# Optimization experiments

Measured on AMD Instinct MI355X. Metric: run time of the kernel, lower is better.

Reference implementation:

```python
import jax, jax.numpy as jnp
import numpy as np

B, S, HID = 4, 2048, 1024
E, K, H = 8, 2, 8          # num_experts, topk, num_heads
DK = HID // H              # head_qk_dim = 128
DV = HID // H              # head_v_dim = 128
CAP = int(S * 1.0)         # capacity_len = int((S*K)/K * capacity)
CHUNK = 64
EPS = 1e-5


def setup_inputs() -> dict:
    key = jax.random.key(0)
    ks = jax.random.split(key, 12)
    std = 0.02  # ~ xavier_uniform with gain 2**-2.5
    return {
        "x": jax.random.normal(ks[0], (B, S, HID), jnp.float32),
        "gate_w": jax.random.normal(ks[1], (E, HID), jnp.float32) * std,
        "q_w": jax.random.normal(ks[2], (HID, HID), jnp.float32) * std,
        "k_w": jax.random.normal(ks[3], (E, HID, HID), jnp.float32) * std,
        "v_w": jax.random.normal(ks[4], (E, HID, HID), jnp.float32) * std,
        "fmq1_w": jax.random.normal(ks[5], (DK, DK), jnp.float32) * std,
        "fmq2_w": jax.random.normal(ks[6], (DK, DK), jnp.float32) * std,
        "fmk1_w": jax.random.normal(ks[7], (DK, DK), jnp.float32) * std,
        "fmk2_w": jax.random.normal(ks[8], (DK, DK), jnp.float32) * std,
        "norm_w": jnp.ones((DV,), jnp.float32),
        "o_w": jax.random.normal(ks[9], (HID, HID), jnp.float32) * std,
    }


def chunk_linear_attn(q, k, v):
    # q,k: (Bt, T, H, DK); v: (Bt, T, H, DV). Causal linear attention, chunked.
    Bt, T, Hh, Dk = q.shape
    Dv = v.shape[-1]
    nc = T // CHUNK
    q = q * (Dk ** -0.5)
    qc = q.reshape(Bt, nc, CHUNK, Hh, Dk).transpose(1, 0, 2, 3, 4)
    kc = k.reshape(Bt, nc, CHUNK, Hh, Dk).transpose(1, 0, 2, 3, 4)
    vc = v.reshape(Bt, nc, CHUNK, Hh, Dv).transpose(1, 0, 2, 3, 4)
    causal = jnp.tril(jnp.ones((CHUNK, CHUNK), q.dtype))
    def step(Sst, qkv):
        qb, kb, vb = qkv  # (Bt, CHUNK, H, D)
        attn = jnp.einsum('bihd,bjhd->bhij', qb, kb) * causal
        intra = jnp.einsum('bhij,bjhe->bihe', attn, vb)
        inter = jnp.einsum('bihd,bhde->bihe', qb, Sst)
        Sst = Sst + jnp.einsum('bjhd,bjhe->bhde', kb, vb)
        return Sst, intra + inter
    S0 = jnp.zeros((Bt, Hh, Dk, Dv), q.dtype)
    _, o = jax.lax.scan(step, S0, (qc, kc, vc))
    return o.transpose(1, 0, 2, 3, 4).reshape(Bt, T, Hh, Dv)


def _forward(x, gate_w, q_w, k_w, v_w, fmq1_w, fmq2_w, fmk1_w, fmk2_w, norm_w, o_w):
    b, s0, d = x.shape
    # ---- routing ----
    logits = jnp.einsum('bsd,ed->bse', x, gate_w)
    scores = jax.nn.softmax(logits.astype(jnp.float32), axis=-1)
    rw, sel = jax.lax.top_k(scores, K)                 # (b, s0, K)
    rw = (rw / rw.sum(-1, keepdims=True)).astype(x.dtype)
    routing_mask = jax.nn.one_hot(sel, E, dtype=jnp.int32).sum(2)  # (b, s0, E)
    # ---- transform: sort-by-(batch,expert), capacity gather ----
    s = s0 * K
    x_rep = jnp.repeat(x, K, axis=1).reshape(b * s, d)  # repeat_interleave over seq
    sel_flat = sel.reshape(b * s).astype(jnp.int32)
    batch_idx = jnp.repeat(jnp.arange(b, dtype=jnp.int32), s)
    combined = batch_idx * E + sel_flat
    sorted_indices = jnp.argsort(combined)              # stable in jax
    x_sorted = x_rep[sorted_indices]
    tokens = routing_mask.sum(axis=1)                   # (b, E) tokens per group
    flat_off = (jnp.cumsum(tokens, axis=1) + (jnp.arange(b, dtype=jnp.int32) * s)[:, None]).reshape(-1)
    starts = jnp.concatenate([jnp.zeros((1,), flat_off.dtype), flat_off[:-1]])
    idx = starts[:, None] + jnp.arange(CAP, dtype=flat_off.dtype)[None, :]
    shift = jnp.maximum(tokens.reshape(-1) - CAP, 0)    # keep last CAP tokens
    tidx = idx + shift[:, None]                         # (b*E, CAP)
    dmask = tidx < flat_off[:, None]
    tidx = jnp.where(dmask, tidx, 0)
    xe = x_sorted[tidx.reshape(-1)].reshape(b * E, CAP, d) * dmask[..., None].astype(x.dtype)
    xe = xe.reshape(b, E, CAP, d).transpose(1, 0, 2, 3)  # (E, b, CAP, d)
    # ---- projections + Hadamard feature maps ----
    q = jnp.einsum('ebtc,kc->ebtk', xe, q_w).reshape(E, b, CAP, H, DK)
    k = jnp.einsum('ebtc,ekc->ebtk', xe, k_w).reshape(E, b, CAP, H, DK)
    v = jnp.einsum('ebtc,ekc->ebtk', xe, v_w).reshape(E, b, CAP, H, DV)
    q = jnp.einsum('...d,kd->...k', q, fmq1_w) * jnp.einsum('...d,kd->...k', q, fmq2_w)
    k = jnp.einsum('...d,kd->...k', k, fmk1_w) * jnp.einsum('...d,kd->...k', k, fmk2_w)
    # ---- causal chunked linear attention per (expert, batch) slot ----
    o = chunk_linear_attn(q.reshape(E * b, CAP, H, DK),
                          k.reshape(E * b, CAP, H, DK),
                          v.reshape(E * b, CAP, H, DV))
    # ---- reconstruct: scatter-add back, undo sort, weighted topk combine ----
    oflat = o.reshape(E, b, CAP, H, DV).transpose(1, 0, 2, 3, 4).reshape(b * E * CAP, H, DV)
    oflat = oflat * dmask.reshape(-1)[:, None, None].astype(o.dtype)
    res = jnp.zeros((b * s, H, DV), o.dtype).at[tidx.reshape(-1)].add(oflat)
    inv = jnp.argsort(sorted_indices)
    restored = res[inv].reshape(b, s0, K, H, DV)
    out = (restored * rw[..., None, None]).sum(axis=2)   # (b, s0, H, DV)
    # RMSNorm over head_v_dim, merge heads, output proj
    out = out * jax.lax.rsqrt(jnp.mean(out * out, axis=-1, keepdims=True) + EPS) * norm_w
    out = out.reshape(b, s0, H * DV)
    return jnp.einsum('bsv,dv->bsd', out, o_w)


def reference(x, gate_w, q_w, k_w, v_w, fmq1_w, fmq2_w, fmk1_w, fmk2_w, norm_w, o_w):
    return _forward(x, gate_w, q_w, k_w, v_w, fmq1_w, fmq2_w, fmk1_w, fmk2_w, norm_w, o_w)
```

## Files before the change

### kernel.cpp

```cpp
#include <hip/hip_runtime.h>
#include <stdint.h>

typedef unsigned short u16;
typedef unsigned int   u32;
typedef __attribute__((ext_vector_type(4))) float f32x4;
typedef __attribute__((ext_vector_type(4))) u32   u32x4;
typedef __attribute__((ext_vector_type(8))) __bf16 bf16x8;

#define MFMA16(a,b,c) __builtin_amdgcn_mfma_f32_16x16x32_bf16((a),(b),(c),0,0,0)

#define QSCALE 0.08838834764831845f
#define RMAX   24576

__device__ __forceinline__ float bf2f(u16 x){ u32 u=((u32)x)<<16; float f; __builtin_memcpy(&f,&u,4); return f; }
__device__ __forceinline__ u16 f2bf(float f){ u32 u; __builtin_memcpy(&u,&f,4); u = u + 0x7FFFu + ((u>>16)&1u); return (u16)(u>>16); }
__device__ __forceinline__ u32 pack2(float a, float b){ return (u32)f2bf(a) | ((u32)f2bf(b)<<16); }

__device__ __forceinline__ void gl_lds(const u16* g, u16* l){
  __builtin_amdgcn_global_load_lds(
      (const __attribute__((address_space(1))) void*)g,
      (__attribute__((address_space(3))) void*)l, 16, 0, 0);
}

#define TSW(row, oct) ((row)*72 + ((((oct) ^ (((row)>>3)&7)))<<3))


__device__ __forceinline__ void cvt_body(const float* __restrict__ s, u16* __restrict__ d,
                                         long n8, int lb, int nb){
  long idx = (long)lb*256 + threadIdx.x;
  long stride = (long)nb*256;
  for (long i=idx; i<n8; i+=stride){
    const float* p = s + i*8;
    f32x4 a = *(const f32x4*)p;
    f32x4 b = *(const f32x4*)(p+4);
    u32x4 o;
    o[0]=pack2(a[0],a[1]); o[1]=pack2(a[2],a[3]); o[2]=pack2(b[0],b[1]); o[3]=pack2(b[2],b[3]);
    *(u32x4*)(d + i*8) = o;
  }
}

__device__ __forceinline__ void route_body(const float* __restrict__ x, const float* __restrict__ gw,
  int* __restrict__ sel, float* __restrict__ rw, u16* __restrict__ xb, int lb)
{
  int w = threadIdx.x>>6, lane = threadIdx.x&63;
  int tok = lb*4 + w;
  const float* xr = x + (size_t)tok*1024 + lane*16;
  f32x4 xv[4];
  #pragma unroll
  for (int q=0;q<4;q++) xv[q] = *(const f32x4*)(xr + q*4);
  {
    u16* xrow = xb + (size_t)tok*1024 + lane*16;
    u32x4 o0, o1;
    o0[0]=pack2(xv[0][0],xv[0][1]); o0[1]=pack2(xv[0][2],xv[0][3]);
    o0[2]=pack2(xv[1][0],xv[1][1]); o0[3]=pack2(xv[1][2],xv[1][3]);
    o1[0]=pack2(xv[2][0],xv[2][1]); o1[1]=pack2(xv[2][2],xv[2][3]);
    o1[2]=pack2(xv[3][0],xv[3][1]); o1[3]=pack2(xv[3][2],xv[3][3]);
    *(u32x4*)xrow     = o0;
    *(u32x4*)(xrow+8) = o1;
  }
  float part[8];
  #pragma unroll
  for (int e=0;e<8;e++){
    const float* g = gw + e*1024 + lane*16;
    float s = 0.f;
    #pragma unroll
    for (int q=0;q<4;q++){
      f32x4 gv = *(const f32x4*)(g + q*4);
      s += xv[q][0]*gv[0] + xv[q][1]*gv[1] + xv[q][2]*gv[2] + xv[q][3]*gv[3];
    }
    part[e]=s;
  }
  #pragma unroll
  for (int e=0;e<8;e++){
    float v = part[e];
    #pragma unroll
    for (int off=32; off>0; off>>=1) v += __shfl_xor(v, off, 64);
    part[e]=v;
  }
  if (lane==0){
    int i0=0; float m0=part[0];
    #pragma unroll
    for (int e=1;e<8;e++) if (part[e]>m0){ m0=part[e]; i0=e; }
    int i1=0; float m1=-3.4e38f;
    #pragma unroll
    for (int e=0;e<8;e++) if (e!=i0 && part[e]>m1){ m1=part[e]; i1=e; }
    sel[tok] = i0 | (i1<<8);
    float e1 = expf(m1-m0);
    float inv = 1.f/(1.f+e1);
    rw[tok*2+0] = inv;
    rw[tok*2+1] = e1*inv;
  }
}

__device__ __forceinline__ void prep_body(
  const float* __restrict__ q_w, const float* __restrict__ k_w,
  const float* __restrict__ fmq1, const float* __restrict__ fmq2,
  const float* __restrict__ fmk1, const float* __restrict__ fmk2,
  u16* __restrict__ wA, u16* __restrict__ wB, int l, u16* shmem)
{
  int gi = l>>3;
  int c0 = (l&7)*128;
  const float* fm; const float* ws; u16* wd;
  if (gi < 8)      { int h=gi;    fm=fmq1; ws=q_w + (size_t)h*131072; wd=wA + (size_t)h*262144; }
  else if (gi < 16){ int h=gi-8;  fm=fmq2; ws=q_w + (size_t)h*131072; wd=wA + (size_t)h*262144 + 131072; }
  else if (gi < 80){ int t=gi-16, e=t>>3, h=t&7; fm=fmk1; ws=k_w + (size_t)(e*8+h)*131072; wd=wB + (size_t)e*2097152 + (size_t)h*262144; }
  else             { int t=gi-80, e=t>>3, h=t&7; fm=fmk2; ws=k_w + (size_t)(e*8+h)*131072; wd=wB + (size_t)e*2097152 + (size_t)h*262144 + 131072; }
  u16* Af = shmem;
  u16* Bf = shmem + 128*136;
  int tid = threadIdx.x;
  for (int i=tid; i<4096; i+=256){
    int row = i>>5, col = (i&31)*4;
    f32x4 v = *(const f32x4*)&fm[row*128 + col];
    u16* dp = &Af[row*136 + col];
    *(u32*)dp     = pack2(v[0],v[1]);
    *(u32*)(dp+2) = pack2(v[2],v[3]);
  }
  for (int i=tid; i<4096; i+=256){
    int dd = i>>5, cq = (i&31)*4;
    f32x4 v = *(const f32x4*)&ws[(size_t)dd*1024 + c0 + cq];
    #pragma unroll
    for (int j=0;j<4;j++){
      int c = cq+j;
      Bf[c*136 + (dd ^ (((c>>2)&3)<<3))] = f2bf(v[j]);
    }
  }
  __syncthreads();
  int lane=tid&63, w=tid>>6, wr=w>>1, wc=w&1, lc=lane&15, lr=lane>>4;
  const f32x4 Z4 = {0.f,0.f,0.f,0.f};
  f32x4 acc[4][4];
  #pragma unroll
  for (int i=0;i<4;i++){
    #pragma unroll
    for (int j=0;j<4;j++) acc[i][j]=Z4;
  }
  #pragma unroll
  for (int kk=0; kk<4; ++kk){
    bf16x8 a[4], b[4];
    #pragma unroll
    for (int mi=0;mi<4;mi++)
      a[mi] = *(const bf16x8*)&Af[(wr*64+mi*16+lc)*136 + kk*32 + lr*8];
    #pragma unroll
    for (int ni=0;ni<4;ni++){
      int c = wc*64+ni*16+lc;
      b[ni] = *(const bf16x8*)&Bf[c*136 + ((kk*32 + lr*8) ^ (((c>>2)&3)<<3))];
    }
    #pragma unroll
    for (int mi=0;mi<4;mi++){
      #pragma unroll
      for (int ni=0;ni<4;ni++)
        acc[mi][ni] = MFMA16(a[mi], b[ni], acc[mi][ni]);
    }
  }
  int r0=lr*4;
  #pragma unroll
  for (int mi=0;mi<4;mi++){
    #pragma unroll
    for (int ni=0;ni<4;ni++){
      int col = c0 + wc*64 + ni*16 + lc;
      #pragma unroll
      for (int r=0;r<4;r++){
        int row = wr*64 + mi*16 + r0 + r;
        wd[(size_t)row*1024 + col] = f2bf(acc[mi][ni][r]);
      }
    }
  }
}

__global__ __launch_bounds__(256) void k_pre(
  const float* __restrict__ x, const float* __restrict__ gw,
  int* __restrict__ sel, float* __restrict__ rw,
  const float* __restrict__ q_w, const float* __restrict__ k_w,
  const float* __restrict__ fmq1, const float* __restrict__ fmq2,
  const float* __restrict__ fmk1, const float* __restrict__ fmk2,
  u16* __restrict__ wA, u16* __restrict__ wB, u16* __restrict__ xb,
  const float* __restrict__ v_w, u16* __restrict__ wVb,
  const float* __restrict__ o_w, u16* __restrict__ wOb, int* __restrict__ done)
{
  __shared__ __align__(16) u16 shmem[2*128*136];
  int bid = blockIdx.x;
  if (bid==0 && threadIdx.x==0) *done = 0;
  if (bid < 2048)      route_body(x, gw, sel, rw, xb, bid);
  else if (bid < 3200) prep_body(q_w, k_w, fmq1, fmq2, fmk1, fmk2, wA, wB, bid-2048, shmem);
  else if (bid < 3456) cvt_body(v_w, wVb, 1048576L, bid-3200, 256);
  else                 cvt_body(o_w, wOb, 131072L, bid-3456, 32);
}

__global__ __launch_bounds__(256) void k_count(const int* __restrict__ sel,
  int* __restrict__ slot_of, int* __restrict__ src_of, int* __restrict__ meta,
  int* __restrict__ done)
{
  int g = blockIdx.x, b = g>>3, e = g&7;
  int tid = threadIdx.x;
  __shared__ int cn[256];
  unsigned char ex[16];
  int cnt=0;
  #pragma unroll
  for (int i=0;i<16;i++){
    int t = tid*16+i;
    int sv = sel[b*2048 + (t>>1)];
    int ee = (t&1) ? ((sv>>8)&255) : (sv&255);
    ex[i]=(unsigned char)ee;
    cnt += (ee==e);
  }
  cn[tid]=cnt;
  __syncthreads();
  for (int off=1; off<256; off<<=1){
    int v = (tid>=off) ? cn[tid-off] : 0;
    __syncthreads();
    cn[tid] += v;
    __syncthreads();
  }
  int total = cn[255];
  int run = cn[tid]-cnt;
  int shift = total>2048 ? total-2048 : 0;
  #pragma unroll
  for (int i=0;i<16;i++){
    int t = tid*16+i;
    if (ex[i]==e){
      int j = run - shift;
      run++;
      slot_of[b*4096 + t] = (j>=0)? j : -1;
      if (j>=0) src_of[g*2048 + j] = t;
    }
  }
  if (tid==0){
    meta[g]=total;
    __threadfence();
    if (atomicAdd(done,1)==31){
      int basev=0, t=0;
      meta[96]=0;
      for (int gg=0; gg<32; ++gg){
        int n = atomicAdd(&meta[gg],0);
        int nact = n<2048 ? n : 2048;
        int npad = (nact+255)&~255;
        meta[32+gg]=nact;
        meta[64+gg]=npad;
        meta[129+gg]=(nact+63)>>6;
        for (int i=0;i<(npad>>8);++i) meta[192+t++]=gg;
        basev += npad;
        meta[97+gg]=basev;
      }
      meta[161]=basev;
    }
  }
}

__global__ __launch_bounds__(256) void k_gather(const u16* __restrict__ xb,
  const int* __restrict__ src_of, const int* __restrict__ meta, u16* __restrict__ xg,
  int* __restrict__ tokmap)
{
  int g = blockIdx.y, jb = blockIdx.x;
  int npad = meta[64+g];
  if (jb*64 >= npad) return;
  int nact = meta[32+g], base = meta[96+g];
  int tid = threadIdx.x;
  int j = jb*64 + (tid>>2);
  int quart = tid&3;
  int src = (j<nact) ? src_of[g*2048+j] : -1;
  int token = (src>=0) ? ((g>>3)*2048 + (src>>1)) : 0;
  if (quart==0) tokmap[base+j] = token;
  u16* orow = xg + ((size_t)(base+j))*1024 + quart*256;
  if (src>=0){
    const u16* xr = xb + (size_t)token*1024 + quart*256;
    #pragma unroll
    for (int i=0;i<256;i+=8) *(u32x4*)(orow+i) = *(const u32x4*)(xr+i);
  } else {
    u32x4 z = {0,0,0,0};
    #pragma unroll
    for (int i=0;i<256;i+=8) *(u32x4*)(orow+i)=z;
  }
}

__global__ __launch_bounds__(512,2) void k_gemmQKV(const u16* __restrict__ xb, const u16* __restrict__ xg,
  const u16* __restrict__ wA, const u16* __restrict__ wB, const u16* __restrict__ wVb,
  u16* __restrict__ qh, u16* __restrict__ kh, u16* __restrict__ vv, const int* __restrict__ meta)
{
  int bid = blockIdx.x;
  int role, tm, tn;
  const u16 *A, *Wp; u16* outB;
  if (bid < 256){
    role=0; int l=bid, xcd=l&7, jj=l>>3, jd=jj>>3;
    tm=xcd*4+jd; tn=jj&7;
    A=xb; Wp=wA + (size_t)tn*262144; outB=qh;
  } else if (bid < 1024){
    role=1; int l=bid-256, xcd=l&7, jj=l>>3, jd=jj>>3;
    tm=xcd*12+jd; tn=jj&7;
    if (tm*256 >= meta[161]) return;
    A=xg; Wp=wB + (size_t)(meta[192+tm]&7)*2097152 + (size_t)tn*262144; outB=kh;
  } else {
    role=2; int l=bid-1024, xcd=l&7, jj=l>>3, jd=jj>>2;
    tm=xcd*12+jd; tn=jj&3;
    if (tm*256 >= meta[161]) return;
    A=xg; Wp=wVb + (size_t)(meta[192+tm]&7)*1048576 + (size_t)tn*262144; outB=vv;
  }

  __shared__ __align__(16) u16 smem[65536];

  int tid=threadIdx.x, lane=tid&63;
  int w=tid>>6, wr=w>>2, wc=w&3, lc=lane&15, lr=lane>>4;
  int swz = lc&7;
  int ck0 = ((lr)^swz)<<3;
  int ck1 = ((4+lr)^swz)<<3;
  int arow = (wr*128 + lc)*64;
  int brow = 16384 + (wc*64 + lc)*64;
  const f32x4 Z4 = {0.f,0.f,0.f,0.f};
  f32x4 acc[8][4];
  #pragma unroll
  for(int i=0;i<8;i++){
    #pragma unroll
    for(int j2=0;j2<4;j2++) acc[i][j2]=Z4;
  }
  int rowlane = tid>>3;
  int gch = ((tid&7)^(rowlane&7))*8;
  const u16* Asrc = A  + (size_t)tm*262144 + (size_t)rowlane*1024 + gch;
  const u16* Bsrc = Wp + (size_t)rowlane*1024 + gch;

  #define STG2(dst, src) { \
    gl_lds((src),         &smem[(dst) + tid*8]); \
    gl_lds((src) + 65536, &smem[(dst) + 4096 + tid*8]); }

  #define RDA(dst, jrow) { \
    dst[0] = *(const bf16x8*)&smem[d + arow + (2*(jrow)  )*1024 + ck0]; \
    dst[1] = *(const bf16x8*)&smem[d + arow + (2*(jrow)+1)*1024 + ck0]; \
    dst[2] = *(const bf16x8*)&smem[d + arow + (2*(jrow)  )*1024 + ck1]; \
    dst[3] = *(const bf16x8*)&smem[d + arow + (2*(jrow)+1)*1024 + ck1]; }

  #define DOMFMA(src, jrow) { \
    __builtin_amdgcn_s_setprio(1); \
    _Pragma("unroll") \
    for (int ni=0;ni<4;ni++){ \
      acc[2*(jrow)  ][ni] = MFMA16(src[0], b0[ni], acc[2*(jrow)  ][ni]); \
      acc[2*(jrow)+1][ni] = MFMA16(src[1], b0[ni], acc[2*(jrow)+1][ni]); } \
    _Pragma("unroll") \
    for (int ni=0;ni<4;ni++){ \
      acc[2*(jrow)  ][ni] = MFMA16(src[2], b1[ni], acc[2*(jrow)  ][ni]); \
      acc[2*(jrow)+1][ni] = MFMA16(src[3], b1[ni], acc[2*(jrow)+1][ni]); } \
    __builtin_amdgcn_s_setprio(0); }

  STG2(16384, Bsrc);
  STG2(24576, Bsrc + 131072);
  STG2(0,     Asrc);
  STG2(8192,  Asrc + 131072);
  STG2(49152, Bsrc + 64);
  STG2(57344, Bsrc + 131072 + 64);

  for (int t=0; t<16; ++t){
    int d = (t&1)<<15;
    bf16x8 b0[4], b1[4], aE[4], aO[4];
    if (t<15) asm volatile("s_waitcnt vmcnt(4)" ::: "memory");
    else      asm volatile("s_waitcnt vmcnt(0)" ::: "memory");
    __builtin_amdgcn_s_barrier();
    #pragma unroll
    for (int ni=0;ni<4;ni++){
      b0[ni] = *(const bf16x8*)&smem[d + brow + ni*1024 + ck0];
      b1[ni] = *(const bf16x8*)&smem[d + brow + ni*1024 + ck1];
    }
    RDA(aE, 0);
    if (t<15) STG2(((t+1)&1)<<15, Asrc + (size_t)(t+1)*64);
    RDA(aO, 1);
    DOMFMA(aE, 0);
    __builtin_amdgcn_s_barrier();
    if (t<15) STG2((((t+1)&1)<<15) + 8192, Asrc + 131072 + (size_t)(t+1)*64);
    RDA(aE, 2);
    DOMFMA(aO, 1);
    __builtin_amdgcn_s_barrier();
    if (t<14) STG2(d + 16384, Bsrc + (size_t)(t+2)*64);
    RDA(aO, 3);
    DOMFMA(aE, 2);
    __builtin_amdgcn_s_barrier();
    if (t<14) STG2(d + 24576, Bsrc + 131072 + (size_t)(t+2)*64);
    DOMFMA(aO, 3);
  }
  #undef STG2
  #undef RDA
  #undef DOMFMA

  __syncthreads();
  if (role < 2){
    if (wc >= 2){
      #pragma unroll
      for (int mi=0;mi<8;mi++){
        #pragma unroll
        for (int ni=0;ni<4;ni++){
          int col = (wc-2)*64 + ni*16 + lc;
          #pragma unroll
          for (int r=0;r<4;r++)
            ((float*)smem)[(wr*128+mi*16+lr*4+r)*128 + col] = acc[mi][ni][r];
        }
      }
    }
    __syncthreads();
    if (wc < 2){
      float scl = (role==0) ? QSCALE : 1.0f;
      #pragma unroll
      for (int mi=0;mi<8;mi++){
        #pragma unroll
        for (int ni=0;ni<4;ni++){
          int col = wc*64 + ni*16 + lc;
          #pragma unroll
          for (int r=0;r<4;r++){
            int row = wr*128+mi*16+lr*4+r;
            float v = acc[mi][ni][r] * ((float*)smem)[row*128 + col] * scl;
            outB[(size_t)(tm*256+row)*1024 + tn*128 + col] = f2bf(v);
          }
        }
      }
    }
  } else {
    #pragma unroll
    for (int mi=0;mi<8;mi++){
      #pragma unroll
      for (int ni=0;ni<4;ni++){
        int col = tn*256 + wc*64 + ni*16 + lc;
        #pragma unroll
        for (int r=0;r<4;r++){
          int row = tm*256 + wr*128 + mi*16 + lr*4 + r;
          outB[(size_t)row*1024 + col] = f2bf(acc[mi][ni][r]);
        }
      }
    }
  }
}

__global__ __launch_bounds__(512) void k_gemmO(const u16* __restrict__ A, const u16* __restrict__ W,
  float* __restrict__ outF)
{
  int tnN = gridDim.x;
  int bid = blockIdx.y*tnN + blockIdx.x;
  int chunk = gridDim.y >> 3;
  int xcd = bid & 7, j = bid >> 3;
  int jd = j / tnN;
  int tm = xcd*chunk + jd;
  int tn = j - jd*tnN;

  __shared__ __align__(16) u16 smem[73728];

  int tid=threadIdx.x, lane=tid&63;
  int w=tid>>6, wr=w>>2, wc=w&3, lc=lane&15, lr=lane>>4;
  int swz = lc&7;
  const f32x4 Z4 = {0.f,0.f,0.f,0.f};
  f32x4 acc[4][4];
  #pragma unroll
  for(int i=0;i<4;i++){
    #pragma unroll
    for(int j2=0;j2<4;j2++) acc[i][j2]=Z4;
  }
  size_t lanoff = (size_t)(tid>>3)*1024 + (size_t)(((tid&7)^((tid>>3)&7))*8);
  const u16* Ag = A + (size_t)tm*131072 + lanoff;
  const u16* Bg = W + (size_t)tn*262144 + lanoff;
  int lo = tid*8;

  #define STAGEO(ao, bo, kt) { \
    const u16* ga = Ag + (kt)*64; const u16* gb = Bg + (kt)*64; \
    gl_lds(ga,                 &smem[(ao) + lo]); \
    gl_lds(ga + (size_t)65536, &smem[(ao) + 4096 + lo]); \
    gl_lds(gb,                  &smem[(bo) + lo]); \
    gl_lds(gb + (size_t)65536,  &smem[(bo) + 4096 + lo]); \
    gl_lds(gb + (size_t)131072, &smem[(bo) + 8192 + lo]); \
    gl_lds(gb + (size_t)196608, &smem[(bo) + 12288 + lo]); }

  STAGEO(0, 24576, 0);
  STAGEO(8192, 40960, 1);
  int cur = 0;
  for (int kt=0; kt<16; ++kt){
    if (kt<15) asm volatile("s_waitcnt vmcnt(6)" ::: "memory");
    else       asm volatile("s_waitcnt vmcnt(0)" ::: "memory");
    __builtin_amdgcn_s_barrier();
    if (kt<14){
      int nid = kt+2; nid -= (nid/3)*3;
      STAGEO(nid*8192, 24576+nid*16384, kt+2);
    }
    int ao = cur*8192, bo = 24576 + cur*16384;
    __builtin_amdgcn_s_setprio(1);
    #pragma unroll
    for (int kk=0; kk<2; ++kk){
      bf16x8 a[4], b[4];
      #pragma unroll
      for (int mi=0;mi<4;mi++){
        int row = wr*64+mi*16+lc;
        a[mi] = *(const bf16x8*)&smem[ao + row*64 + (((kk*4+lr)^swz)<<3)];
      }
      #pragma unroll
      for (int ni=0;ni<4;ni++){
        int row = wc*64+ni*16+lc;
        b[ni] = *(const bf16x8*)&smem[bo + row*64 + (((kk*4+lr)^swz)<<3)];
      }
      #pragma unroll
      for (int mi=0;mi<4;mi++){
        #pragma unroll
        for (int ni=0;ni<4;ni++)
          acc[mi][ni] = MFMA16(a[mi], b[ni], acc[mi][ni]);
      }
    }
    __builtin_amdgcn_s_setprio(0);
    cur = (cur==2)?0:cur+1;
  }
  #pragma unroll
  for (int mi=0;mi<4;mi++){
    #pragma unroll
    for (int ni=0;ni<4;ni++){
      int col = tn*256 + wc*64 + ni*16 + lc;
      #pragma unroll
      for (int r=0;r<4;r++){
        int row = tm*128 + wr*64 + mi*16 + lr*4 + r;
        outF[(size_t)row*1024 + col] = acc[mi][ni][r];
      }
    }
  }
  #undef STAGEO
}

__global__ __launch_bounds__(256,1) void k_attn(const u16* __restrict__ qv, const u16* __restrict__ kv,
  const u16* __restrict__ vv, u16* __restrict__ o, const int* __restrict__ meta,
  const int* __restrict__ tokmap)
{
  int g = blockIdx.x>>3, h = blockIdx.x&7;
  int nch = meta[129+g];
  if (nch==0) return;
  int base = meta[96+g];
  __shared__ __align__(16) u16 Qs[64*136];
  __shared__ __align__(16) u16 Ks[64*136];
  __shared__ __align__(16) u16 KTs[128*72];
  __shared__ __align__(16) u16 VTs[128*72];
  __shared__ __align__(16) u16 Ts[2*128*136];
  __shared__ __align__(16) u16 Ps[64*72];
  int tid=threadIdx.x, w=tid>>6, lane=tid&63;
  int wr=w>>1, wc=w&1;
  int lr=lane>>4, lc=lane&15;
  {
    u32x4 z={0,0,0,0};
    for (int i=tid; i<128*136/8; i+=256) *(u32x4*)&Ts[i*8]=z;
  }
  const f32x4 Z4 = {0.f,0.f,0.f,0.f};
  f32x4 accT[4][4];
  #pragma unroll
  for (int i=0;i<4;i++){
    #pragma unroll
    for (int j=0;j<4;j++) accT[i][j]=Z4;
  }
  __syncthreads();
  const u16* kb = kv + (size_t)base*1024 + h*128;
  const u16* vb = vv + (size_t)base*1024 + h*128;
  u16* ob = o + (size_t)base*1024 + h*128;
  int tso = 0;

  for (int c=0; c<nch; ++c){
    #pragma unroll
    for (int it=0; it<4; ++it){
      int id = tid + it*256;
      int row = id>>4, kc = id&15;
      int tok = tokmap[base + c*64 + row];
      *(u32x4*)&Qs[row*136 + kc*8] = *(const u32x4*)(qv + (size_t)tok*1024 + h*128 + kc*8);
      *(u32x4*)&Ks[row*136 + kc*8] = *(const u32x4*)(kb + (size_t)(c*64+row)*1024 + kc*8);
    }
    #pragma unroll
    for (int it=0; it<4; ++it){
      int id = tid + it*256;
      int j = id>>4, dg = id&15;
      int col = (((j>>3) ^ (dg&7))<<3) + (j&7);
      u32x4 kx = *(const u32x4*)(kb + (size_t)(c*64+j)*1024 + dg*8);
      u32x4 vx = *(const u32x4*)(vb + (size_t)(c*64+j)*1024 + dg*8);
      #pragma unroll
      for (int t=0;t<4;t++){
        KTs[(dg*8+t*2  )*72 + col] = (u16)(kx[t]&0xffff);
        KTs[(dg*8+t*2+1)*72 + col] = (u16)(kx[t]>>16);
        VTs[(dg*8+t*2  )*72 + col] = (u16)(vx[t]&0xffff);
        VTs[(dg*8+t*2+1)*72 + col] = (u16)(vx[t]>>16);
      }
    }
    __syncthreads();
    bf16x8 qf[2][4];
    #pragma unroll
    for (int ti=0; ti<2; ++ti){
      #pragma unroll
      for (int ks=0; ks<4; ++ks)
        qf[ti][ks] = *(const bf16x8*)&Qs[(wr*32+ti*16+lc)*136 + ks*32 + lr*8];
    }
    f32x4 accO[2][4];
    #pragma unroll
    for (int i=0;i<2;i++){
      #pragma unroll
      for (int j=0;j<4;j++) accO[i][j]=Z4;
    }
    #pragma unroll
    for (int ks=0; ks<4; ++ks){
      bf16x8 bt[4];
      #pragma unroll
      for (int te=0; te<4; ++te)
        bt[te] = *(const bf16x8*)&Ts[tso + (wc*64+te*16+lc)*136 + ks*32 + lr*8];
      #pragma unroll
      for (int ti=0; ti<2; ++ti){
        #pragma unroll
        for (int te=0; te<4; ++te)
          accO[ti][te] = MFMA16(qf[ti][ks], bt[te], accO[ti][te]);
      }
    }
    f32x4 accP[2][2];
    #pragma unroll
    for (int i=0;i<2;i++){
      #pragma unroll
      for (int j=0;j<2;j++) accP[i][j]=Z4;
    }
    #pragma unroll
    for (int ks=0; ks<4; ++ks){
      bf16x8 bk[2];
      #pragma unroll
      for (int tj=0; tj<2; ++tj)
        bk[tj] = *(const bf16x8*)&Ks[(wc*32+tj*16+lc)*136 + ks*32 + lr*8];
      #pragma unroll
      for (int ti=0; ti<2; ++ti){
        #pragma unroll
        for (int tj=0; tj<2; ++tj)
          accP[ti][tj] = MFMA16(qf[ti][ks], bk[tj], accP[ti][tj]);
      }
    }
    #pragma unroll
    for (int ti=0; ti<2; ++ti){
      #pragma unroll
      for (int tj=0; tj<2; ++tj){
        #pragma unroll
        for (int r=0;r<4;r++){
          int i = wr*32+ti*16+lr*4+r;
          int j = wc*32+tj*16+lc;
          Ps[i*72 + j] = f2bf( (j<=i) ? accP[ti][tj][r] : 0.f );
        }
      }
    }
    __syncthreads();
    #pragma unroll
    for (int ks=0; ks<2; ++ks){
      bf16x8 ap[2], bv[4];
      #pragma unroll
      for (int ti=0; ti<2; ++ti)
        ap[ti] = *(const bf16x8*)&Ps[(wr*32+ti*16+lc)*72 + ks*32 + lr*8];
      #pragma unroll
      for (int te=0; te<4; ++te)
        bv[te] = *(const bf16x8*)&VTs[TSW(wc*64+te*16+lc, ks*4+lr)];
      #pragma unroll
      for (int ti=0; ti<2; ++ti){
        #pragma unroll
        for (int te=0; te<4; ++te)
          accO[ti][te] = MFMA16(ap[ti], bv[te], accO[ti][te]);
      }
    }
    #pragma unroll
    for (int ks=0; ks<2; ++ks){
      bf16x8 av[4], bk2[4];
      #pragma unroll
      for (int te=0; te<4; ++te)
        av[te] = *(const bf16x8*)&VTs[TSW(wr*64+te*16+lc, ks*4+lr)];
      #pragma unroll
      for (int td=0; td<4; ++td)
        bk2[td] = *(const bf16x8*)&KTs[TSW(wc*64+td*16+lc, ks*4+lr)];
      #pragma unroll
      for (int te=0; te<4; ++te){
        #pragma unroll
        for (int td=0; td<4; ++td)
          accT[te][td] = MFMA16(av[te], bk2[td], accT[te][td]);
      }
    }
    int tsn = tso ^ (128*136);
    #pragma unroll
    for (int te=0; te<4; ++te){
      #pragma unroll
      for (int td=0; td<4; ++td){
        int dk = wc*64+td*16+lc;
        #pragma unroll
        for (int r=0;r<4;r++){
          int erow = wr*64+te*16+lr*4+r;
          Ts[tsn + erow*136 + dk] = f2bf(accT[te][td][r]);
        }
      }
    }
    #pragma unroll
    for (int ti=0; ti<2; ++ti){
      #pragma unroll
      for (int te=0; te<4; ++te){
        int ecol = wc*64+te*16+lc;
        #pragma unroll
        for (int r=0;r<4;r++){
          int i = wr*32+ti*16+lr*4+r;
          ob[(size_t)(c*64+i)*1024 + ecol] = f2bf(accO[ti][te][r]);
        }
      }
    }
    __syncthreads();
    tso = tsn;
  }
}

__global__ __launch_bounds__(256) void k_comb(const u16* __restrict__ o, const int* __restrict__ sel,
  const float* __restrict__ rw, const int* __restrict__ slot_of, const int* __restrict__ meta,
  const float* __restrict__ nw, u16* __restrict__ fin)
{
  int w=threadIdx.x>>6, lane=threadIdx.x&63;
  int tok = blockIdx.x*4 + w;
  int b = tok>>11;
  int sv = sel[tok];
  float acc[16];
  #pragma unroll
  for (int i=0;i<16;i++) acc[i]=0.f;
  #pragma unroll
  for (int kk=0; kk<2; ++kk){
    int e = kk ? ((sv>>8)&255) : (sv&255);
    int j = slot_of[tok*2 + kk];
    if (j < 0) continue;
    float wgt = rw[tok*2+kk];
    int row = meta[96 + b*8 + e] + j;
    const u16* orow = o + (size_t)row*1024 + lane*16;
    #pragma unroll
    for (int q=0;q<2;q++){
      u32x4 v = *(const u32x4*)(orow + q*8);
      #pragma unroll
      for (int t=0;t<4;t++){
        acc[q*8+t*2]   += wgt * bf2f((u16)(v[t]&0xffff));
        acc[q*8+t*2+1] += wgt * bf2f((u16)(v[t]>>16));
      }
    }
  }
  float ssq=0.f;
  #pragma unroll
  for (int i=0;i<16;i++) ssq += acc[i]*acc[i];
  ssq += __shfl_xor(ssq,1,64);
  ssq += __shfl_xor(ssq,2,64);
  ssq += __shfl_xor(ssq,4,64);
  float sc = rsqrtf(ssq*(1.f/128.f) + 1e-5f);
  int cbase = (lane&7)*16;
  u32x4 o0, o1;
  #pragma unroll
  for (int t=0;t<4;t++)
    o0[t] = pack2(acc[2*t]*sc*nw[cbase+2*t], acc[2*t+1]*sc*nw[cbase+2*t+1]);
  #pragma unroll
  for (int t=0;t<4;t++)
    o1[t] = pack2(acc[8+2*t]*sc*nw[cbase+8+2*t], acc[8+2*t+1]*sc*nw[cbase+8+2*t+1]);
  u16* fp = fin + (size_t)tok*1024 + lane*16;
  *(u32x4*)fp     = o0;
  *(u32x4*)(fp+8) = o1;
}

extern "C" void kernel_launch(void* const* d_in, const int* in_sizes, int n_in,
                              void* d_out, int out_size, void* d_ws, size_t ws_size,
                              hipStream_t stream)
{
  (void)in_sizes; (void)n_in;
  const float* x     = (const float*)d_in[0];
  const float* gate  = (const float*)d_in[1];
  const float* q_w   = (const float*)d_in[2];
  const float* k_w   = (const float*)d_in[3];
  const float* v_w   = (const float*)d_in[4];
  const float* fmq1  = (const float*)d_in[5];
  const float* fmq2  = (const float*)d_in[6];
  const float* fmk1  = (const float*)d_in[7];
  const float* fmk2  = (const float*)d_in[8];
  const float* norm_w= (const float*)d_in[9];
  const float* o_w   = (const float*)d_in[10];
  float* out = (float*)d_out;

  uint8_t* ws = (uint8_t*)d_ws;
  size_t off = 0;
  auto alloc = [&](size_t bytes)->void*{ void* p = ws + off; off += (bytes + 255) & ~(size_t)255; return p; };
  int*   meta = (int*)alloc(4096);
  int*   sel  = (int*)alloc(8192*4);
  float* rwb  = (float*)alloc(8192*2*4);
  int*   slot = (int*)alloc(16384*4);
  int*   srcf = (int*)alloc((size_t)32*2048*4);
  int*   tokm = (int*)alloc((size_t)RMAX*4);
  int*   done = (int*)alloc(256);
  u16* wA  = (u16*)alloc((size_t)2097152*2);
  u16* wVb = (u16*)alloc((size_t)8388608*2);
  u16* wOb = (u16*)alloc((size_t)1048576*2);
  u16* xb  = (u16*)alloc((size_t)8192*1024*2);
  u16* xg  = (u16*)alloc((size_t)RMAX*1024*2);
  u16* qh  = (u16*)alloc((size_t)8192*1024*2);
  u16* kh  = (u16*)alloc((size_t)RMAX*1024*2);
  u16* vv  = (u16*)alloc((size_t)RMAX*1024*2);
  if (off > ws_size){
    hipMemsetAsync(d_out, 0x7F, (size_t)out_size*4, stream);
    return;
  }
  u16* wB  = (u16*)d_out;
  u16* ob  = xg;
  u16* fin = qh;

  k_pre<<<3488,256,0,stream>>>(x, gate, sel, rwb, q_w, k_w, fmq1, fmq2, fmk1, fmk2, wA, wB, xb, v_w, wVb, o_w, wOb, done);
  k_count<<<32,256,0,stream>>>(sel, slot, srcf, meta, done);
  k_gather<<<dim3(32,32),256,0,stream>>>(xb, srcf, meta, xg, tokm);
  k_gemmQKV<<<1408,512,0,stream>>>(xb, xg, wA, wB, wVb, qh, kh, vv, meta);
  k_attn<<<256,256,0,stream>>>(qh, kh, vv, ob, meta, tokm);
  k_comb<<<2048,256,0,stream>>>(ob, sel, rwb, slot, meta, norm_w, fin);
  k_gemmO<<<dim3(4,64),512,0,stream>>>(fin, wOb, out);
}
```

Measured before the change: 404.3 us.

## Fuse token gather into QKV GEMM loads and share weight staging in prep

```diff
diff --git a/kernel.cpp b/kernel.cpp
--- a/kernel.cpp
+++ b/kernel.cpp
@@ -98,24 +98,23 @@
   const float* __restrict__ fmk1, const float* __restrict__ fmk2,
   u16* __restrict__ wA, u16* __restrict__ wB, int l, u16* shmem)
 {
-  int gi = l>>3;
-  int c0 = (l&7)*128;
-  const float* fm; const float* ws; u16* wd;
-  if (gi < 8)      { int h=gi;    fm=fmq1; ws=q_w + (size_t)h*131072; wd=wA + (size_t)h*262144; }
-  else if (gi < 16){ int h=gi-8;  fm=fmq2; ws=q_w + (size_t)h*131072; wd=wA + (size_t)h*262144 + 131072; }
-  else if (gi < 80){ int t=gi-16, e=t>>3, h=t&7; fm=fmk1; ws=k_w + (size_t)(e*8+h)*131072; wd=wB + (size_t)e*2097152 + (size_t)h*262144; }
-  else             { int t=gi-80, e=t>>3, h=t&7; fm=fmk2; ws=k_w + (size_t)(e*8+h)*131072; wd=wB + (size_t)e*2097152 + (size_t)h*262144 + 131072; }
+  const float *fm1, *fm2, *ws; u16 *wd1;
+  int c0;
+  if (l < 64){
+    int h = l>>3; c0 = (l&7)*128;
+    fm1=fmq1; fm2=fmq2; ws=q_w + (size_t)h*131072;
+    wd1=wA + (size_t)h*262144;
+  } else {
+    int l2=l-64, eh=l2>>3; c0=(l2&7)*128;
+    int e=eh>>3, h=eh&7;
+    fm1=fmk1; fm2=fmk2; ws=k_w + (size_t)eh*131072;
+    wd1=wB + (size_t)e*2097152 + (size_t)h*262144;
+  }
+  u16* wd2 = wd1 + 131072;
   u16* Af = shmem;
   u16* Bf = shmem + 128*136;
   int tid = threadIdx.x;
   for (int i=tid; i<4096; i+=256){
-    int row = i>>5, col = (i&31)*4;
-    f32x4 v = *(const f32x4*)&fm[row*128 + col];
-    u16* dp = &Af[row*136 + col];
-    *(u32*)dp     = pack2(v[0],v[1]);
-    *(u32*)(dp+2) = pack2(v[2],v[3]);
-  }
-  for (int i=tid; i<4096; i+=256){
     int dd = i>>5, cq = (i&31)*4;
     f32x4 v = *(const f32x4*)&ws[(size_t)dd*1024 + c0 + cq];
     #pragma unroll
@@ -124,45 +123,58 @@
       Bf[c*136 + (dd ^ (((c>>2)&3)<<3))] = f2bf(v[j]);
     }
   }
-  __syncthreads();
   int lane=tid&63, w=tid>>6, wr=w>>1, wc=w&1, lc=lane&15, lr=lane>>4;
   const f32x4 Z4 = {0.f,0.f,0.f,0.f};
-  f32x4 acc[4][4];
-  #pragma unroll
-  for (int i=0;i<4;i++){
-    #pragma unroll
-    for (int j=0;j<4;j++) acc[i][j]=Z4;
-  }
-  #pragma unroll
-  for (int kk=0; kk<4; ++kk){
-    bf16x8 a[4], b[4];
-    #pragma unroll
-    for (int mi=0;mi<4;mi++)
-      a[mi] = *(const bf16x8*)&Af[(wr*64+mi*16+lc)*136 + kk*32 + lr*8];
-    #pragma unroll
-    for (int ni=0;ni<4;ni++){
-      int c = wc*64+ni*16+lc;
-      b[ni] = *(const bf16x8*)&Bf[c*136 + ((kk*32 + lr*8) ^ (((c>>2)&3)<<3))];
-    }
+  #pragma unroll
+  for (int pass=0; pass<2; ++pass){
+    const float* fm = pass ? fm2 : fm1;
+    u16* wd = pass ? wd2 : wd1;
+    for (int i=tid; i<4096; i+=256){
+      int row = i>>5, col = (i&31)*4;
+      f32x4 v = *(const f32x4*)&fm[row*128 + col];
+      u16* dp = &Af[row*136 + col];
+      *(u32*)dp     = pack2(v[0],v[1]);
+      *(u32*)(dp+2) = pack2(v[2],v[3]);
+    }
+    __syncthreads();
+    f32x4 acc[4][4];
+    #pragma unroll
+    for (int i=0;i<4;i++){
+      #pragma unroll
+      for (int j=0;j<4;j++) acc[i][j]=Z4;
+    }
+    #pragma unroll
+    for (int kk=0; kk<4; ++kk){
+      bf16x8 a[4], b[4];
+      #pragma unroll
+      for (int mi=0;mi<4;mi++)
+        a[mi] = *(const bf16x8*)&Af[(wr*64+mi*16+lc)*136 + kk*32 + lr*8];
+      #pragma unroll
+      for (int ni=0;ni<4;ni++){
+        int c = wc*64+ni*16+lc;
+        b[ni] = *(const bf16x8*)&Bf[c*136 + ((kk*32 + lr*8) ^ (((c>>2)&3)<<3))];
+      }
+      #pragma unroll
+      for (int mi=0;mi<4;mi++){
+        #pragma unroll
+        for (int ni=0;ni<4;ni++)
+          acc[mi][ni] = MFMA16(a[mi], b[ni], acc[mi][ni]);
+      }
+    }
+    int r0=lr*4;
     #pragma unroll
     for (int mi=0;mi<4;mi++){
       #pragma unroll
-      for (int ni=0;ni<4;ni++)
-        acc[mi][ni] = MFMA16(a[mi], b[ni], acc[mi][ni]);
-    }
-  }
-  int r0=lr*4;
-  #pragma unroll
-  for (int mi=0;mi<4;mi++){
-    #pragma unroll
-    for (int ni=0;ni<4;ni++){
-      int col = c0 + wc*64 + ni*16 + lc;
-      #pragma unroll
-      for (int r=0;r<4;r++){
-        int row = wr*64 + mi*16 + r0 + r;
-        wd[(size_t)row*1024 + col] = f2bf(acc[mi][ni][r]);
-      }
-    }
+      for (int ni=0;ni<4;ni++){
+        int col = c0 + wc*64 + ni*16 + lc;
+        #pragma unroll
+        for (int r=0;r<4;r++){
+          int row = wr*64 + mi*16 + r0 + r;
+          wd[(size_t)row*1024 + col] = f2bf(acc[mi][ni][r]);
+        }
+      }
+    }
+    __syncthreads();
   }
 }
 
@@ -180,13 +192,19 @@
   int bid = blockIdx.x;
   if (bid==0 && threadIdx.x==0) *done = 0;
   if (bid < 2048)      route_body(x, gw, sel, rw, xb, bid);
-  else if (bid < 3200) prep_body(q_w, k_w, fmq1, fmq2, fmk1, fmk2, wA, wB, bid-2048, shmem);
-  else if (bid < 3456) cvt_body(v_w, wVb, 1048576L, bid-3200, 256);
-  else                 cvt_body(o_w, wOb, 131072L, bid-3456, 32);
+  else if (bid < 2624) prep_body(q_w, k_w, fmq1, fmq2, fmk1, fmk2, wA, wB, bid-2048, shmem);
+  else if (bid < 2880) cvt_body(v_w, wVb, 1048576L, bid-2624, 256);
+  else if (bid < 2912) cvt_body(o_w, wOb, 131072L, bid-2880, 32);
+  else {
+    if (threadIdx.x < 128){
+      u32x4 z = {0,0,0,0};
+      *(u32x4*)&xb[(size_t)8192*1024 + threadIdx.x*8] = z;
+    }
+  }
 }
 
 __global__ __launch_bounds__(256) void k_count(const int* __restrict__ sel,
-  int* __restrict__ slot_of, int* __restrict__ src_of, int* __restrict__ meta,
+  int* __restrict__ slot_of, int* __restrict__ tokmap2, int* __restrict__ meta,
   int* __restrict__ done)
 {
   int g = blockIdx.x, b = g>>3, e = g&7;
@@ -220,7 +238,7 @@
       int j = run - shift;
       run++;
       slot_of[b*4096 + t] = (j>=0)? j : -1;
-      if (j>=0) src_of[g*2048 + j] = t;
+      if (j>=0) tokmap2[g*2048 + j] = b*2048 + (t>>1);
     }
   }
   if (tid==0){
@@ -245,53 +263,28 @@
   }
 }
 
-__global__ __launch_bounds__(256) void k_gather(const u16* __restrict__ xb,
-  const int* __restrict__ src_of, const int* __restrict__ meta, u16* __restrict__ xg,
-  int* __restrict__ tokmap)
-{
-  int g = blockIdx.y, jb = blockIdx.x;
-  int npad = meta[64+g];
-  if (jb*64 >= npad) return;
-  int nact = meta[32+g], base = meta[96+g];
-  int tid = threadIdx.x;
-  int j = jb*64 + (tid>>2);
-  int quart = tid&3;
-  int src = (j<nact) ? src_of[g*2048+j] : -1;
-  int token = (src>=0) ? ((g>>3)*2048 + (src>>1)) : 0;
-  if (quart==0) tokmap[base+j] = token;
-  u16* orow = xg + ((size_t)(base+j))*1024 + quart*256;
-  if (src>=0){
-    const u16* xr = xb + (size_t)token*1024 + quart*256;
-    #pragma unroll
-    for (int i=0;i<256;i+=8) *(u32x4*)(orow+i) = *(const u32x4*)(xr+i);
-  } else {
-    u32x4 z = {0,0,0,0};
-    #pragma unroll
-    for (int i=0;i<256;i+=8) *(u32x4*)(orow+i)=z;
-  }
-}
-
-__global__ __launch_bounds__(512,2) void k_gemmQKV(const u16* __restrict__ xb, const u16* __restrict__ xg,
+__global__ __launch_bounds__(512,2) void k_gemmQKV(const u16* __restrict__ xb,
   const u16* __restrict__ wA, const u16* __restrict__ wB, const u16* __restrict__ wVb,
-  u16* __restrict__ qh, u16* __restrict__ kh, u16* __restrict__ vv, const int* __restrict__ meta)
+  u16* __restrict__ qh, u16* __restrict__ kh, u16* __restrict__ vv,
+  const int* __restrict__ meta, const int* __restrict__ tokmap2)
 {
   int bid = blockIdx.x;
   int role, tm, tn;
-  const u16 *A, *Wp; u16* outB;
+  const u16 *Wp; u16* outB;
   if (bid < 256){
     role=0; int l=bid, xcd=l&7, jj=l>>3, jd=jj>>3;
     tm=xcd*4+jd; tn=jj&7;
-    A=xb; Wp=wA + (size_t)tn*262144; outB=qh;
+    Wp=wA + (size_t)tn*262144; outB=qh;
   } else if (bid < 1024){
     role=1; int l=bid-256, xcd=l&7, jj=l>>3, jd=jj>>3;
     tm=xcd*12+jd; tn=jj&7;
     if (tm*256 >= meta[161]) return;
-    A=xg; Wp=wB + (size_t)(meta[192+tm]&7)*2097152 + (size_t)tn*262144; outB=kh;
+    Wp=wB + (size_t)(meta[192+tm]&7)*2097152 + (size_t)tn*262144; outB=kh;
   } else {
     role=2; int l=bid-1024, xcd=l&7, jj=l>>3, jd=jj>>2;
     tm=xcd*12+jd; tn=jj&3;
     if (tm*256 >= meta[161]) return;
-    A=xg; Wp=wVb + (size_t)(meta[192+tm]&7)*1048576 + (size_t)tn*262144; outB=vv;
+    Wp=wVb + (size_t)(meta[192+tm]&7)*1048576 + (size_t)tn*262144; outB=vv;
   }
 
   __shared__ __align__(16) u16 smem[65536];
@@ -312,10 +305,31 @@
   }
   int rowlane = tid>>3;
   int gch = ((tid&7)^(rowlane&7))*8;
-  const u16* Asrc = A  + (size_t)tm*262144 + (size_t)rowlane*1024 + gch;
+  int tk0, tk1, tk2, tk3;
+  {
+    int r0 = tm*256 + rowlane;
+    if (role==0){
+      tk0=r0; tk1=r0+64; tk2=r0+128; tk3=r0+192;
+    } else {
+      int g = meta[192+tm], base = meta[96+g], nact = meta[32+g];
+      int gb = g*2048;
+      int j0 = r0 - base;
+      tk0 = (j0     < nact) ? tokmap2[gb + j0]     : 8192;
+      tk1 = (j0+64  < nact) ? tokmap2[gb + j0+64]  : 8192;
+      tk2 = (j0+128 < nact) ? tokmap2[gb + j0+128] : 8192;
+      tk3 = (j0+192 < nact) ? tokmap2[gb + j0+192] : 8192;
+    }
+  }
+  const u16* Ap0 = xb + (size_t)tk0*1024 + gch;
+  const u16* Ap1 = xb + (size_t)tk1*1024 + gch;
+  const u16* Ap2 = xb + (size_t)tk2*1024 + gch;
+  const u16* Ap3 = xb + (size_t)tk3*1024 + gch;
   const u16* Bsrc = Wp + (size_t)rowlane*1024 + gch;
 
-  #define STG2(dst, src) { \
+  #define STGA(dst, p0, p1, coff) { \
+    gl_lds((p0) + (coff), &smem[(dst) + tid*8]); \
+    gl_lds((p1) + (coff), &smem[(dst) + 4096 + tid*8]); }
+  #define STGB(dst, src) { \
     gl_lds((src),         &smem[(dst) + tid*8]); \
     gl_lds((src) + 65536, &smem[(dst) + 4096 + tid*8]); }
 
@@ -337,12 +351,12 @@
       acc[2*(jrow)+1][ni] = MFMA16(src[3], b1[ni], acc[2*(jrow)+1][ni]); } \
     __builtin_amdgcn_s_setprio(0); }
 
-  STG2(16384, Bsrc);
-  STG2(24576, Bsrc + 131072);
-  STG2(0,     Asrc);
-  STG2(8192,  Asrc + 131072);
-  STG2(49152, Bsrc + 64);
-  STG2(57344, Bsrc + 131072 + 64);
+  STGB(16384, Bsrc);
+  STGB(24576, Bsrc + 131072);
+  STGA(0,     Ap0, Ap1, 0);
+  STGA(8192,  Ap2, Ap3, 0);
+  STGB(49152, Bsrc + 64);
+  STGB(57344, Bsrc + 131072 + 64);
 
   for (int t=0; t<16; ++t){
     int d = (t&1)<<15;
@@ -356,22 +370,23 @@
       b1[ni] = *(const bf16x8*)&smem[d + brow + ni*1024 + ck1];
     }
     RDA(aE, 0);
-    if (t<15) STG2(((t+1)&1)<<15, Asrc + (size_t)(t+1)*64);
+    if (t<15) STGA(((t+1)&1)<<15, Ap0, Ap1, (size_t)(t+1)*64);
     RDA(aO, 1);
     DOMFMA(aE, 0);
     __builtin_amdgcn_s_barrier();
-    if (t<15) STG2((((t+1)&1)<<15) + 8192, Asrc + 131072 + (size_t)(t+1)*64);
+    if (t<15) STGA((((t+1)&1)<<15) + 8192, Ap2, Ap3, (size_t)(t+1)*64);
     RDA(aE, 2);
     DOMFMA(aO, 1);
     __builtin_amdgcn_s_barrier();
-    if (t<14) STG2(d + 16384, Bsrc + (size_t)(t+2)*64);
+    if (t<14) STGB(d + 16384, Bsrc + (size_t)(t+2)*64);
     RDA(aO, 3);
     DOMFMA(aE, 2);
     __builtin_amdgcn_s_barrier();
-    if (t<14) STG2(d + 24576, Bsrc + 131072 + (size_t)(t+2)*64);
+    if (t<14) STGB(d + 24576, Bsrc + 131072 + (size_t)(t+2)*64);
     DOMFMA(aO, 3);
   }
-  #undef STG2
+  #undef STGA
+  #undef STGB
   #undef RDA
   #undef DOMFMA
 
@@ -512,12 +527,12 @@
 
 __global__ __launch_bounds__(256,1) void k_attn(const u16* __restrict__ qv, const u16* __restrict__ kv,
   const u16* __restrict__ vv, u16* __restrict__ o, const int* __restrict__ meta,
-  const int* __restrict__ tokmap)
+  const int* __restrict__ tokmap2)
 {
   int g = blockIdx.x>>3, h = blockIdx.x&7;
   int nch = meta[129+g];
   if (nch==0) return;
-  int base = meta[96+g];
+  int base = meta[96+g], nact = meta[32+g];
   __shared__ __align__(16) u16 Qs[64*136];
   __shared__ __align__(16) u16 Ks[64*136];
   __shared__ __align__(16) u16 KTs[128*72];
@@ -549,23 +564,20 @@
     for (int it=0; it<4; ++it){
       int id = tid + it*256;
       int row = id>>4, kc = id&15;
-      int tok = tokmap[base + c*64 + row];
-      *(u32x4*)&Qs[row*136 + kc*8] = *(const u32x4*)(qv + (size_t)tok*1024 + h*128 + kc*8);
-      *(u32x4*)&Ks[row*136 + kc*8] = *(const u32x4*)(kb + (size_t)(c*64+row)*1024 + kc*8);
-    }
-    #pragma unroll
-    for (int it=0; it<4; ++it){
-      int id = tid + it*256;
-      int j = id>>4, dg = id&15;
-      int col = (((j>>3) ^ (dg&7))<<3) + (j&7);
-      u32x4 kx = *(const u32x4*)(kb + (size_t)(c*64+j)*1024 + dg*8);
-      u32x4 vx = *(const u32x4*)(vb + (size_t)(c*64+j)*1024 + dg*8);
+      int jj = c*64 + row;
+      int tok = tokmap2[g*2048 + (jj<nact ? jj : 0)];
+      u32x4 qx = *(const u32x4*)(qv + (size_t)tok*1024 + h*128 + kc*8);
+      u32x4 kx = *(const u32x4*)(kb + (size_t)jj*1024 + kc*8);
+      u32x4 vx = *(const u32x4*)(vb + (size_t)jj*1024 + kc*8);
+      *(u32x4*)&Qs[row*136 + kc*8] = qx;
+      *(u32x4*)&Ks[row*136 + kc*8] = kx;
+      int col = (((row>>3) ^ (kc&7))<<3) + (row&7);
       #pragma unroll
       for (int t=0;t<4;t++){
-        KTs[(dg*8+t*2  )*72 + col] = (u16)(kx[t]&0xffff);
-        KTs[(dg*8+t*2+1)*72 + col] = (u16)(kx[t]>>16);
-        VTs[(dg*8+t*2  )*72 + col] = (u16)(vx[t]&0xffff);
-        VTs[(dg*8+t*2+1)*72 + col] = (u16)(vx[t]>>16);
+        KTs[(kc*8+t*2  )*72 + col] = (u16)(kx[t]&0xffff);
+        KTs[(kc*8+t*2+1)*72 + col] = (u16)(kx[t]>>16);
+        VTs[(kc*8+t*2  )*72 + col] = (u16)(vx[t]&0xffff);
+        VTs[(kc*8+t*2+1)*72 + col] = (u16)(vx[t]>>16);
       }
     }
     __syncthreads();
@@ -763,14 +775,13 @@
   int*   sel  = (int*)alloc(8192*4);
   float* rwb  = (float*)alloc(8192*2*4);
   int*   slot = (int*)alloc(16384*4);
-  int*   srcf = (int*)alloc((size_t)32*2048*4);
-  int*   tokm = (int*)alloc((size_t)RMAX*4);
+  int*   tokm2= (int*)alloc((size_t)65536*4);
   int*   done = (int*)alloc(256);
   u16* wA  = (u16*)alloc((size_t)2097152*2);
   u16* wVb = (u16*)alloc((size_t)8388608*2);
   u16* wOb = (u16*)alloc((size_t)1048576*2);
-  u16* xb  = (u16*)alloc((size_t)8192*1024*2);
-  u16* xg  = (u16*)alloc((size_t)RMAX*1024*2);
+  u16* xb  = (u16*)alloc((size_t)8193*1024*2);
+  u16* ob  = (u16*)alloc((size_t)RMAX*1024*2);
   u16* qh  = (u16*)alloc((size_t)8192*1024*2);
   u16* kh  = (u16*)alloc((size_t)RMAX*1024*2);
   u16* vv  = (u16*)alloc((size_t)RMAX*1024*2);
@@ -779,14 +790,12 @@
     return;
   }
   u16* wB  = (u16*)d_out;
-  u16* ob  = xg;
   u16* fin = qh;
 
-  k_pre<<<3488,256,0,stream>>>(x, gate, sel, rwb, q_w, k_w, fmq1, fmq2, fmk1, fmk2, wA, wB, xb, v_w, wVb, o_w, wOb, done);
-  k_count<<<32,256,0,stream>>>(sel, slot, srcf, meta, done);
-  k_gather<<<dim3(32,32),256,0,stream>>>(xb, srcf, meta, xg, tokm);
-  k_gemmQKV<<<1408,512,0,stream>>>(xb, xg, wA, wB, wVb, qh, kh, vv, meta);
-  k_attn<<<256,256,0,stream>>>(qh, kh, vv, ob, meta, tokm);
+  k_pre<<<2913,256,0,stream>>>(x, gate, sel, rwb, q_w, k_w, fmq1, fmq2, fmk1, fmk2, wA, wB, xb, v_w, wVb, o_w, wOb, done);
+  k_count<<<32,256,0,stream>>>(sel, slot, tokm2, meta, done);
+  k_gemmQKV<<<1408,512,0,stream>>>(xb, wA, wB, wVb, qh, kh, vv, meta, tokm2);
+  k_attn<<<256,256,0,stream>>>(qh, kh, vv, ob, meta, tokm2);
   k_comb<<<2048,256,0,stream>>>(ob, sel, rwb, slot, meta, norm_w, fin);
   k_gemmO<<<dim3(4,64),512,0,stream>>>(fin, wOb, out);
 }
```

After: 345.9 us. 14.4% less time.
